# Optimization experiments

Measured on AMD Instinct MI355X. Metric: run time of the kernel, lower is better.

## Reference

```python
import jax, jax.numpy as jnp
import numpy as np

B = 16384      # batch
F = 26         # onehot fields
E = 32         # embedding_dim
L = 50         # multihot bag length
V = 1000000    # num_embeddings
CT = 13        # continuous features
D0, D1, D2, D3 = 909, 512, 256, 1
LEAKY = 0.01


def _leaky(x):
    return jnp.where(x >= 0, x, LEAKY * x)


def setup_inputs() -> dict:
    key = jax.random.key(0)
    ks = jax.random.split(key, 16)
    inp = {
        "onehot_i": jax.random.randint(ks[0], (B, F), 0, V),
        "onehot_x": jax.random.uniform(ks[1], (B, F), dtype=jnp.float32),
        "multihot_i1": jax.random.randint(ks[2], (B, L), 0, V),
        "multihot_x1": jax.random.uniform(ks[3], (B, L), dtype=jnp.float32),
        "multihot_i2": jax.random.randint(ks[4], (B, L), 0, V),
        "multihot_x2": jax.random.uniform(ks[5], (B, L), dtype=jnp.float32),
        "ctns": jax.random.normal(ks[6], (B, CT), dtype=jnp.float32),
        # learned parameters
        "wide_table": jax.random.normal(ks[7], (V, 1), dtype=jnp.float32) * 0.02,
        "deep_table": jax.random.normal(ks[8], (V, E), dtype=jnp.float32) * 0.02,
        "w2": jax.random.normal(ks[9], (D1, D0), dtype=jnp.float32) * (1.0 / np.sqrt(D0)),
        "b2": jnp.zeros((D1,), dtype=jnp.float32),
        "w3": jax.random.normal(ks[10], (D2, D1), dtype=jnp.float32) * (1.0 / np.sqrt(D1)),
        "b3": jnp.zeros((D2,), dtype=jnp.float32),
        "w4": jax.random.normal(ks[11], (D3, D2), dtype=jnp.float32) * (1.0 / np.sqrt(D2)),
        "b4": jnp.zeros((D3,), dtype=jnp.float32),
    }
    return inp


def reference(onehot_i, onehot_x, multihot_i1, multihot_x1, multihot_i2,
              multihot_x2, ctns, wide_table, deep_table, w2, b2, w3, b3, w4, b4):
    # ---- wide part ----
    # Original broadcasts the [B,F,1] wide embedding against x repeated E times,
    # then sums over all columns. That equals E * sum_f(w[idx]*x).
    wide_sum = (wide_table[onehot_i, 0] * onehot_x).sum(axis=1)          # [B]
    wide_sum = wide_sum + (wide_table[multihot_i1, 0] * multihot_x1).sum(axis=1)
    wide_sum = wide_sum + (wide_table[multihot_i2, 0] * multihot_x2).sum(axis=1)
    wide_out = E * wide_sum                                              # [B]

    # ---- deep part: gather, scale by field weight, pool multihot bags ----
    d_one = (deep_table[onehot_i] * onehot_x[:, :, None]).reshape(B, F * E)   # [B, F*E]
    d_m1 = (deep_table[multihot_i1] * multihot_x1[:, :, None]).sum(axis=1)    # [B, E]
    d_m2 = (deep_table[multihot_i2] * multihot_x2[:, :, None]).sum(axis=1)    # [B, E]
    x = jnp.concatenate([d_one, d_m1, d_m2, ctns], axis=1)                    # [B, D0]

    # dropout p=0.0 (deterministic reference)
    x = _leaky(x @ w2.T + b2)
    x = _leaky(x @ w3.T + b3)
    x = (x @ w4.T + b4).squeeze(-1)                                           # [B]
    return jax.nn.sigmoid(x + wide_out)
```

## Files before the change

### kernel.cpp

```cpp
#include <hip/hip_runtime.h>
#include <hip/hip_bf16.h>
#include <math.h>

#define B_    16384
#define F_    26
#define E_    32
#define L_    50
#define CT_   13
#define D0_   909
#define D0P   928
#define D1_   512
#define D2_   256

#define NEMB  4096
#define W2N   (D1_ * D0P)
#define W3N   (D2_ * D1_)
#define CVTB  ((W2N + W3N + 255) / 256)

typedef __bf16 bf16x8 __attribute__((ext_vector_type(8)));
typedef float f32x4 __attribute__((ext_vector_type(4)));

__device__ inline unsigned short f2b(float f) {
    union { __hip_bfloat16 h; unsigned short u; } v;
    v.h = __float2bfloat16(f);
    return v.u;
}
__device__ inline void gld_lds16(const void* g, void* l) {
    __builtin_amdgcn_global_load_lds(
        (const __attribute__((address_space(1))) unsigned int*)g,
        (__attribute__((address_space(3))) unsigned int*)l, 16, 0, 0);
}

__global__ __launch_bounds__(256) void embed_cvt_kernel(
    const int* __restrict__ oi, const float* __restrict__ ox,
    const int* __restrict__ i1, const float* __restrict__ x1,
    const int* __restrict__ i2, const float* __restrict__ x2,
    const float* __restrict__ ct, const float* __restrict__ wtab,
    const float* __restrict__ dtab,
    const float* __restrict__ w2, const float* __restrict__ w3,
    __hip_bfloat16* __restrict__ x0b, float* __restrict__ wid,
    __hip_bfloat16* __restrict__ w2b, __hip_bfloat16* __restrict__ w3b)
{
    const int tid  = threadIdx.x;
    const int lane = tid & 63;
    const int w    = tid >> 6;

    if (blockIdx.x >= NEMB) {
        int i = (blockIdx.x - NEMB) * 256 + tid;
        if (i < W2N) {
            int r = i / D0P, c = i - r * D0P;
            float v = (c < D0_) ? w2[r * D0_ + c] : 0.f;
            w2b[i] = __float2bfloat16(v);
        } else {
            int j = i - W2N;
            if (j < W3N) w3b[j] = __float2bfloat16(w3[j]);
        }
        return;
    }

    const int s = blockIdx.x * 4 + w;
    const int g = lane >> 3;
    const int l = lane & 7;
    unsigned short* xrow = (unsigned short*)(x0b + (size_t)s * D0P);
    const f32x4* dt4 = (const f32x4*)dtab;

    int koh[4]; float soh[4];
#pragma unroll
    for (int t = 0; t < 4; t++) {
        int f = g + 8 * t; bool v = (f < F_);
        koh[t] = v ? oi[s * F_ + f] : 0;
        soh[t] = v ? ox[s * F_ + f] : 0.f;
    }
    int k1[7], k2[7]; float sc1[7], sc2[7];
#pragma unroll
    for (int t = 0; t < 7; t++) {
        int j = g + 8 * t; bool v = (j < L_);
        k1[t]  = v ? i1[s * L_ + j] : 0;
        sc1[t] = v ? x1[s * L_ + j] : 0.f;
        k2[t]  = v ? i2[s * L_ + j] : 0;
        sc2[t] = v ? x2[s * L_ + j] : 0.f;
    }
    f32x4 r1[7], r2[7], roh[4];
#pragma unroll
    for (int t = 0; t < 7; t++) r1[t] = dt4[(size_t)k1[t] * 8 + l];
#pragma unroll
    for (int t = 0; t < 7; t++) r2[t] = dt4[(size_t)k2[t] * 8 + l];
#pragma unroll
    for (int t = 0; t < 4; t++) roh[t] = dt4[(size_t)koh[t] * 8 + l];

#pragma unroll
    for (int t = 0; t < 4; t++) {
        int f = g + 8 * t;
        if (f < F_) {
            ushort4 o;
            o.x = f2b(roh[t].x * soh[t]); o.y = f2b(roh[t].y * soh[t]);
            o.z = f2b(roh[t].z * soh[t]); o.w = f2b(roh[t].w * soh[t]);
            *(ushort4*)(xrow + f * E_ + l * 4) = o;
        }
    }
    f32x4 a1 = {0.f,0.f,0.f,0.f}, a2 = {0.f,0.f,0.f,0.f};
#pragma unroll
    for (int t = 0; t < 7; t++) {
        a1.x = fmaf(r1[t].x, sc1[t], a1.x); a1.y = fmaf(r1[t].y, sc1[t], a1.y);
        a1.z = fmaf(r1[t].z, sc1[t], a1.z); a1.w = fmaf(r1[t].w, sc1[t], a1.w);
        a2.x = fmaf(r2[t].x, sc2[t], a2.x); a2.y = fmaf(r2[t].y, sc2[t], a2.y);
        a2.z = fmaf(r2[t].z, sc2[t], a2.z); a2.w = fmaf(r2[t].w, sc2[t], a2.w);
    }
#pragma unroll
    for (int m = 8; m < 64; m <<= 1) {
        a1.x += __shfl_xor(a1.x, m); a1.y += __shfl_xor(a1.y, m);
        a1.z += __shfl_xor(a1.z, m); a1.w += __shfl_xor(a1.w, m);
        a2.x += __shfl_xor(a2.x, m); a2.y += __shfl_xor(a2.y, m);
        a2.z += __shfl_xor(a2.z, m); a2.w += __shfl_xor(a2.w, m);
    }
    if (g == 0) {
        ushort4 o; o.x = f2b(a1.x); o.y = f2b(a1.y); o.z = f2b(a1.z); o.w = f2b(a1.w);
        *(ushort4*)(xrow + F_ * E_ + l * 4) = o;
    }
    if (g == 1) {
        ushort4 o; o.x = f2b(a2.x); o.y = f2b(a2.y); o.z = f2b(a2.z); o.w = f2b(a2.w);
        *(ushort4*)(xrow + F_ * E_ + E_ + l * 4) = o;
    }
    if (lane < E_) {
        float v = (lane < CT_) ? ct[s * CT_ + lane] : 0.f;
        xrow[F_ * E_ + 2 * E_ + lane] = f2b(v);
    }
    float acc = 0.f;
#pragma unroll
    for (int t = lane; t < F_ + 2 * L_; t += 64) {
        int idx; float xv;
        if (t < F_)            { idx = oi[s * F_ + t];           xv = ox[s * F_ + t]; }
        else if (t < F_ + L_)  { int j = t - F_;      idx = i1[s * L_ + j]; xv = x1[s * L_ + j]; }
        else                   { int j = t - F_ - L_; idx = i2[s * L_ + j]; xv = x2[s * L_ + j]; }
        acc += wtab[idx] * xv;
    }
    for (int o = 32; o; o >>= 1) acc += __shfl_xor(acc, o);
    if (lane == 0) wid[s] = (float)E_ * acc;
}

__global__ __launch_bounds__(256) void gemm1_kernel(
    const __hip_bfloat16* __restrict__ A,
    const __hip_bfloat16* __restrict__ W,
    const float* __restrict__ bias,
    __hip_bfloat16* __restrict__ C)
{
    __shared__ __hip_bfloat16 As[128 * 32];
    __shared__ __hip_bfloat16 Bs[128 * 32];

    const int bm   = blockIdx.x & 127;
    const int bn   = blockIdx.x >> 7;
    const int tid  = threadIdx.x;
    const int lane = tid & 63;
    const int w    = tid >> 6;
    const int wm   = w >> 1, wn = w & 1;

    f32x4 acc[4][4] = {};

    const int srow = lane >> 2;
    const int scol = (lane & 3) * 8;
    const __hip_bfloat16* Aw0 = A + ((size_t)bm * 128 + w * 32 + srow) * D0P + scol;
    const __hip_bfloat16* Aw1 = Aw0 + (size_t)16 * D0P;
    const __hip_bfloat16* Ww0 = W + ((size_t)bn * 128 + w * 32 + srow) * D0P + scol;
    const __hip_bfloat16* Ww1 = Ww0 + (size_t)16 * D0P;
    char* AsW = (char*)As + w * 2048;
    char* BsW = (char*)Bs + w * 2048;

    const int fr = lane & 15;
    const int kg = (lane >> 4) * 8;

    for (int k0 = 0; k0 < D0P; k0 += 32) {
        gld_lds16(Aw0 + k0, AsW);
        gld_lds16(Aw1 + k0, AsW + 1024);
        gld_lds16(Ww0 + k0, BsW);
        gld_lds16(Ww1 + k0, BsW + 1024);
        __syncthreads();

        bf16x8 af[4], bfv[4];
#pragma unroll
        for (int i = 0; i < 4; i++)
            af[i] = *(const bf16x8*)(As + (wm * 64 + i * 16 + fr) * 32 + kg);
#pragma unroll
        for (int i = 0; i < 4; i++)
            bfv[i] = *(const bf16x8*)(Bs + (wn * 64 + i * 16 + fr) * 32 + kg);
#pragma unroll
        for (int i = 0; i < 4; i++)
#pragma unroll
            for (int j = 0; j < 4; j++)
                acc[i][j] = __builtin_amdgcn_mfma_f32_16x16x32_bf16(af[i], bfv[j], acc[i][j], 0, 0, 0);
        __syncthreads();
    }

    float bv[4];
#pragma unroll
    for (int j = 0; j < 4; j++) bv[j] = bias[bn * 128 + wn * 64 + j * 16 + fr];
    const int crow0 = bm * 128 + wm * 64 + (lane >> 4) * 4;
    const int ccol0 = bn * 128 + wn * 64 + fr;
#pragma unroll
    for (int i = 0; i < 4; i++)
#pragma unroll
        for (int j = 0; j < 4; j++)
#pragma unroll
            for (int r = 0; r < 4; r++) {
                float v = acc[i][j][r] + bv[j];
                v = (v >= 0.f) ? v : 0.01f * v;
                C[(size_t)(crow0 + i * 16 + r) * D1_ + ccol0 + j * 16] = __float2bfloat16(v);
            }
}

__global__ __launch_bounds__(256) void g2f_kernel(
    const __hip_bfloat16* __restrict__ h1b, const __hip_bfloat16* __restrict__ w3b,
    const float* __restrict__ b3, const float* __restrict__ w4,
    const float* __restrict__ b4, const float* __restrict__ wid,
    float* __restrict__ out)
{
    __shared__ __align__(16) char smem[21504];
    const int tid  = threadIdx.x;
    const int lane = tid & 63;
    const int w    = tid >> 6;
    const int r0   = blockIdx.x * 64;

    __hip_bfloat16* As2 = (__hip_bfloat16*)smem;
    __hip_bfloat16* Bs2 = (__hip_bfloat16*)(smem + 4096);
    float* parts        = (float*)(smem + 20480);

    f32x4 acc[4][4] = {};
    const int srow = lane >> 2;
    const int scol = (lane & 3) * 8;
    const int fr = lane & 15;
    const int kg = (lane >> 4) * 8;

    for (int ks = 0; ks < 16; ks++) {
        gld_lds16(h1b + ((size_t)r0 + w * 16 + srow) * D1_ + ks * 32 + scol,
                  smem + w * 1024);
#pragma unroll
        for (int rr = 0; rr < 4; rr++)
            gld_lds16(w3b + ((size_t)w * 64 + rr * 16 + srow) * D1_ + ks * 32 + scol,
                      smem + 4096 + w * 4096 + rr * 1024);
        __syncthreads();
        bf16x8 af[4], bfv[4];
#pragma unroll
        for (int i = 0; i < 4; i++)
            af[i] = *(const bf16x8*)(As2 + (i * 16 + fr) * 32 + kg);
#pragma unroll
        for (int j = 0; j < 4; j++)
            bfv[j] = *(const bf16x8*)(Bs2 + (w * 64 + j * 16 + fr) * 32 + kg);
#pragma unroll
        for (int i = 0; i < 4; i++)
#pragma unroll
            for (int j = 0; j < 4; j++)
                acc[i][j] = __builtin_amdgcn_mfma_f32_16x16x32_bf16(af[i], bfv[j], acc[i][j], 0, 0, 0);
        __syncthreads();
    }

    float p[4][4];
#pragma unroll
    for (int i = 0; i < 4; i++)
#pragma unroll
        for (int r = 0; r < 4; r++) p[i][r] = 0.f;
#pragma unroll
    for (int j = 0; j < 4; j++) {
        int n = w * 64 + j * 16 + fr;
        float bb = b3[n];
        float wv = w4[n];
#pragma unroll
        for (int i = 0; i < 4; i++)
#pragma unroll
            for (int r = 0; r < 4; r++) {
                float v = acc[i][j][r] + bb;
                v = (v >= 0.f) ? v : 0.01f * v;
                p[i][r] = fmaf(v, wv, p[i][r]);
            }
    }
#pragma unroll
    for (int m = 1; m < 16; m <<= 1)
#pragma unroll
        for (int i = 0; i < 4; i++)
#pragma unroll
            for (int r = 0; r < 4; r++) p[i][r] += __shfl_xor(p[i][r], m);
    if (fr == 0) {
        int kq = lane >> 4;
#pragma unroll
        for (int i = 0; i < 4; i++)
#pragma unroll
            for (int r = 0; r < 4; r++)
                parts[w * 64 + i * 16 + kq * 4 + r] = p[i][r];
    }
    __syncthreads();
    if (tid < 64) {
        float x = parts[tid] + parts[64 + tid] + parts[128 + tid] + parts[192 + tid]
                + b4[0] + wid[r0 + tid];
        out[r0 + tid] = 1.f / (1.f + expf(-x));
    }
}

extern "C" void kernel_launch(void* const* d_in, const int* in_sizes, int n_in,
                              void* d_out, int out_size, void* d_ws, size_t ws_size,
                              hipStream_t stream) {
    const int*   oi  = (const int*)  d_in[0];
    const float* ox  = (const float*)d_in[1];
    const int*   i1  = (const int*)  d_in[2];
    const float* x1  = (const float*)d_in[3];
    const int*   i2  = (const int*)  d_in[4];
    const float* x2  = (const float*)d_in[5];
    const float* ct  = (const float*)d_in[6];
    const float* wt  = (const float*)d_in[7];
    const float* dt  = (const float*)d_in[8];
    const float* w2  = (const float*)d_in[9];
    const float* b2  = (const float*)d_in[10];
    const float* w3  = (const float*)d_in[11];
    const float* b3  = (const float*)d_in[12];
    const float* w4  = (const float*)d_in[13];
    const float* b4  = (const float*)d_in[14];
    float* out = (float*)d_out;

    char* ws = (char*)d_ws;
    __hip_bfloat16* x0b = (__hip_bfloat16*)(ws);
    __hip_bfloat16* h1b = (__hip_bfloat16*)(ws + 30408704);
    float*          wid = (float*)         (ws + 47185920);
    __hip_bfloat16* w2b = (__hip_bfloat16*)(ws + 47251456);
    __hip_bfloat16* w3b = (__hip_bfloat16*)(ws + 48201728);

    embed_cvt_kernel<<<NEMB + CVTB, 256, 0, stream>>>(
        oi, ox, i1, x1, i2, x2, ct, wt, dt, w2, w3, x0b, wid, w2b, w3b);
    gemm1_kernel<<<512, 256, 0, stream>>>(x0b, w2b, b2, h1b);
    g2f_kernel<<<256, 256, 0, stream>>>(h1b, w3b, b3, w4, b4, wid, out);
}
```

Measured before the change: 119.2 us.

## Fuse both MLP GEMMs into one kernel keeping hidden activations in LDS

Merges the first-layer GEMM and the second-layer GEMM plus final dot into a single kernel where each 512-thread block computes a 64-row slice through all layers. The 512-wide hidden activations stay in padded shared memory instead of being written to and reread from global memory, and one kernel launch is removed. In exchange, each block rereads the whole W2 and W3 weights, with lower tile reuse than the prior 128x128 tiling, and the large LDS footprint allows only one block per CU.

```diff
diff --git a/kernel.cpp b/kernel.cpp
--- a/kernel.cpp
+++ b/kernel.cpp
@@ -138,112 +138,46 @@
     if (lane == 0) wid[s] = (float)E_ * acc;
 }
 
-__global__ __launch_bounds__(256) void gemm1_kernel(
-    const __hip_bfloat16* __restrict__ A,
-    const __hip_bfloat16* __restrict__ W,
-    const float* __restrict__ bias,
-    __hip_bfloat16* __restrict__ C)
+__global__ __launch_bounds__(512, 2) void mlp_kernel(
+    const __hip_bfloat16* __restrict__ x0b,
+    const __hip_bfloat16* __restrict__ w2b, const float* __restrict__ b2,
+    const __hip_bfloat16* __restrict__ w3b, const float* __restrict__ b3,
+    const float* __restrict__ w4, const float* __restrict__ b4,
+    const float* __restrict__ wid, float* __restrict__ out)
 {
-    __shared__ __hip_bfloat16 As[128 * 32];
-    __shared__ __hip_bfloat16 Bs[128 * 32];
-
-    const int bm   = blockIdx.x & 127;
-    const int bn   = blockIdx.x >> 7;
-    const int tid  = threadIdx.x;
-    const int lane = tid & 63;
-    const int w    = tid >> 6;
-    const int wm   = w >> 1, wn = w & 1;
-
-    f32x4 acc[4][4] = {};
-
-    const int srow = lane >> 2;
-    const int scol = (lane & 3) * 8;
-    const __hip_bfloat16* Aw0 = A + ((size_t)bm * 128 + w * 32 + srow) * D0P + scol;
-    const __hip_bfloat16* Aw1 = Aw0 + (size_t)16 * D0P;
-    const __hip_bfloat16* Ww0 = W + ((size_t)bn * 128 + w * 32 + srow) * D0P + scol;
-    const __hip_bfloat16* Ww1 = Ww0 + (size_t)16 * D0P;
-    char* AsW = (char*)As + w * 2048;
-    char* BsW = (char*)Bs + w * 2048;
-
-    const int fr = lane & 15;
-    const int kg = (lane >> 4) * 8;
-
-    for (int k0 = 0; k0 < D0P; k0 += 32) {
-        gld_lds16(Aw0 + k0, AsW);
-        gld_lds16(Aw1 + k0, AsW + 1024);
-        gld_lds16(Ww0 + k0, BsW);
-        gld_lds16(Ww1 + k0, BsW + 1024);
-        __syncthreads();
-
-        bf16x8 af[4], bfv[4];
-#pragma unroll
-        for (int i = 0; i < 4; i++)
-            af[i] = *(const bf16x8*)(As + (wm * 64 + i * 16 + fr) * 32 + kg);
-#pragma unroll
-        for (int i = 0; i < 4; i++)
-            bfv[i] = *(const bf16x8*)(Bs + (wn * 64 + i * 16 + fr) * 32 + kg);
-#pragma unroll
-        for (int i = 0; i < 4; i++)
-#pragma unroll
-            for (int j = 0; j < 4; j++)
-                acc[i][j] = __builtin_amdgcn_mfma_f32_16x16x32_bf16(af[i], bfv[j], acc[i][j], 0, 0, 0);
-        __syncthreads();
-    }
-
-    float bv[4];
-#pragma unroll
-    for (int j = 0; j < 4; j++) bv[j] = bias[bn * 128 + wn * 64 + j * 16 + fr];
-    const int crow0 = bm * 128 + wm * 64 + (lane >> 4) * 4;
-    const int ccol0 = bn * 128 + wn * 64 + fr;
-#pragma unroll
-    for (int i = 0; i < 4; i++)
-#pragma unroll
-        for (int j = 0; j < 4; j++)
-#pragma unroll
-            for (int r = 0; r < 4; r++) {
-                float v = acc[i][j][r] + bv[j];
-                v = (v >= 0.f) ? v : 0.01f * v;
-                C[(size_t)(crow0 + i * 16 + r) * D1_ + ccol0 + j * 16] = __float2bfloat16(v);
-            }
-}
-
-__global__ __launch_bounds__(256) void g2f_kernel(
-    const __hip_bfloat16* __restrict__ h1b, const __hip_bfloat16* __restrict__ w3b,
-    const float* __restrict__ b3, const float* __restrict__ w4,
-    const float* __restrict__ b4, const float* __restrict__ wid,
-    float* __restrict__ out)
-{
-    __shared__ __align__(16) char smem[21504];
+    __shared__ __align__(16) __hip_bfloat16 stageA[64 * 32];
+    __shared__ __align__(16) __hip_bfloat16 stageB[512 * 32];
+    __shared__ __align__(16) unsigned short h1s[16 * 64 * 40];
+    __shared__ float parts[8 * 64];
+
     const int tid  = threadIdx.x;
     const int lane = tid & 63;
     const int w    = tid >> 6;
     const int r0   = blockIdx.x * 64;
-
-    __hip_bfloat16* As2 = (__hip_bfloat16*)smem;
-    __hip_bfloat16* Bs2 = (__hip_bfloat16*)(smem + 4096);
-    float* parts        = (float*)(smem + 20480);
-
-    f32x4 acc[4][4] = {};
+    const int fr   = lane & 15;
+    const int kq   = lane >> 4;
+    const int kg8  = kq * 8;
     const int srow = lane >> 2;
     const int scol = (lane & 3) * 8;
-    const int fr = lane & 15;
-    const int kg = (lane >> 4) * 8;
-
-    for (int ks = 0; ks < 16; ks++) {
-        gld_lds16(h1b + ((size_t)r0 + w * 16 + srow) * D1_ + ks * 32 + scol,
-                  smem + w * 1024);
-#pragma unroll
-        for (int rr = 0; rr < 4; rr++)
-            gld_lds16(w3b + ((size_t)w * 64 + rr * 16 + srow) * D1_ + ks * 32 + scol,
-                      smem + 4096 + w * 4096 + rr * 1024);
+
+    f32x4 acc[4][4] = {};
+    for (int ks = 0; ks < 29; ks++) {
+        if (lane < 32)
+            gld_lds16(x0b + (size_t)(r0 + w * 8 + (lane >> 2)) * D0P + ks * 32 + scol,
+                      (char*)stageA + w * 512);
+#pragma unroll
+        for (int r = 0; r < 4; r++)
+            gld_lds16(w2b + (size_t)(w * 64 + r * 16 + srow) * D0P + ks * 32 + scol,
+                      (char*)stageB + w * 4096 + r * 1024);
         __syncthreads();
+
         bf16x8 af[4], bfv[4];
 #pragma unroll
         for (int i = 0; i < 4; i++)
-            af[i] = *(const bf16x8*)(As2 + (i * 16 + fr) * 32 + kg);
+            af[i] = *(const bf16x8*)(stageA + (i * 16 + fr) * 32 + kg8);
 #pragma unroll
         for (int j = 0; j < 4; j++)
-            bfv[j] = *(const bf16x8*)(Bs2 + (w * 64 + j * 16 + fr) * 32 + kg);
+            bfv[j] = *(const bf16x8*)(stageB + (w * 64 + j * 16 + fr) * 32 + kg8);
 #pragma unroll
         for (int i = 0; i < 4; i++)
 #pragma unroll
@@ -252,21 +186,62 @@
         __syncthreads();
     }
 
+#pragma unroll
+    for (int j = 0; j < 4; j++) {
+        const int n   = w * 64 + j * 16 + fr;
+        const float bb = b2[n];
+        const int ksl = w * 2 + (j >> 1);
+        const int kk  = (j & 1) * 16 + fr;
+#pragma unroll
+        for (int i = 0; i < 4; i++)
+#pragma unroll
+            for (int r = 0; r < 4; r++) {
+                const int row = i * 16 + kq * 4 + r;
+                float v = acc[i][j][r] + bb;
+                v = (v >= 0.f) ? v : 0.01f * v;
+                h1s[ksl * 2560 + row * 40 + kk] = f2b(v);
+            }
+    }
+    __syncthreads();
+
+    f32x4 acc2[4][2] = {};
+    for (int ks = 0; ks < 16; ks++) {
+#pragma unroll
+        for (int r = 0; r < 2; r++)
+            gld_lds16(w3b + (size_t)(w * 32 + r * 16 + srow) * D1_ + ks * 32 + scol,
+                      (char*)stageB + w * 2048 + r * 1024);
+        __syncthreads();
+
+        bf16x8 af[4], bfv[2];
+#pragma unroll
+        for (int i = 0; i < 4; i++)
+            af[i] = *(const bf16x8*)(h1s + ks * 2560 + (i * 16 + fr) * 40 + kg8);
+#pragma unroll
+        for (int j = 0; j < 2; j++)
+            bfv[j] = *(const bf16x8*)(stageB + (w * 32 + j * 16 + fr) * 32 + kg8);
+#pragma unroll
+        for (int i = 0; i < 4; i++)
+#pragma unroll
+            for (int j = 0; j < 2; j++)
+                acc2[i][j] = __builtin_amdgcn_mfma_f32_16x16x32_bf16(af[i], bfv[j], acc2[i][j], 0, 0, 0);
+        __syncthreads();
+    }
+
     float p[4][4];
 #pragma unroll
     for (int i = 0; i < 4; i++)
 #pragma unroll
         for (int r = 0; r < 4; r++) p[i][r] = 0.f;
 #pragma unroll
-    for (int j = 0; j < 4; j++) {
-        int n = w * 64 + j * 16 + fr;
-        float bb = b3[n];
-        float wv = w4[n];
+    for (int j = 0; j < 2; j++) {
+        const int n = w * 32 + j * 16 + fr;
+        const float bb = b3[n];
+        const float wv = w4[n];
 #pragma unroll
         for (int i = 0; i < 4; i++)
 #pragma unroll
             for (int r = 0; r < 4; r++) {
-                float v = acc[i][j][r] + bb;
+                float v = acc2[i][j][r] + bb;
                 v = (v >= 0.f) ? v : 0.01f * v;
                 p[i][r] = fmaf(v, wv, p[i][r]);
             }
@@ -278,7 +253,6 @@
 #pragma unroll
             for (int r = 0; r < 4; r++) p[i][r] += __shfl_xor(p[i][r], m);
     if (fr == 0) {
-        int kq = lane >> 4;
 #pragma unroll
         for (int i = 0; i < 4; i++)
 #pragma unroll
@@ -287,8 +261,9 @@
     }
     __syncthreads();
     if (tid < 64) {
-        float x = parts[tid] + parts[64 + tid] + parts[128 + tid] + parts[192 + tid]
-                + b4[0] + wid[r0 + tid];
+        float x = b4[0] + wid[r0 + tid];
+#pragma unroll
+        for (int ww = 0; ww < 8; ww++) x += parts[ww * 64 + tid];
         out[r0 + tid] = 1.f / (1.f + expf(-x));
     }
 }
@@ -315,13 +290,11 @@
 
     char* ws = (char*)d_ws;
     __hip_bfloat16* x0b = (__hip_bfloat16*)(ws);
-    __hip_bfloat16* h1b = (__hip_bfloat16*)(ws + 30408704);
-    float*          wid = (float*)         (ws + 47185920);
-    __hip_bfloat16* w2b = (__hip_bfloat16*)(ws + 47251456);
-    __hip_bfloat16* w3b = (__hip_bfloat16*)(ws + 48201728);
+    float*          wid = (float*)         (ws + 30408704);
+    __hip_bfloat16* w2b = (__hip_bfloat16*)(ws + 30474240);
+    __hip_bfloat16* w3b = (__hip_bfloat16*)(ws + 31424512);
 
     embed_cvt_kernel<<<NEMB + CVTB, 256, 0, stream>>>(
         oi, ox, i1, x1, i2, x2, ct, wt, dt, w2, w3, x0b, wid, w2b, w3b);
-    gemm1_kernel<<<512, 256, 0, stream>>>(x0b, w2b, b2, h1b);
-    g2f_kernel<<<256, 256, 0, stream>>>(h1b, w3b, b3, w4, b4, wid, out);
-}
+    mlp_kernel<<<B_ / 64, 512, 0, stream>>>(x0b, w2b, b2, w3b, b3, w4, b4, wid, out);
+}
```

Result: slower. 126.2 us (+5.9%).
